# Optimization experiments

Hardware: AMD Instinct MI355X
Metric: run time of the kernel (lower is better)

## Reference

```python
import jax, jax.numpy as jnp
import numpy as np

B, RES, C = 32, 56, 128
HEADS, WS, NW = 4, 7, 8
HD = C // HEADS            # 32
NQ = NW * NW               # 64 windows
WA = WS * WS               # 49 tokens per window
TOPK = 64


def _topk_closest(q_win, k_win, topk):
    qh, qw = q_win; kh, kw = k_win
    ch_q = np.arange(qh); cw_q = np.arange(qw)
    if qh != kh:
        f = kh // qh
        ch_q = ch_q * f + f // 2
        cw_q = cw_q * f + f // 2
    cq = np.stack(np.meshgrid(ch_q, cw_q, indexing='ij'))              # (2,qh,qw)
    ck = np.stack(np.meshgrid(np.arange(kh), np.arange(kw), indexing='ij'))
    fq = cq.reshape(2, -1); fk = ck.reshape(2, -1)
    rel = fq[:, :, None] - fk[:, None, :]                               # (2,nQ,nK)
    dist = np.sqrt(rel[0].astype(np.float32) ** 2 + rel[1].astype(np.float32) ** 2)
    topk = min(topk, dist.shape[1])
    idx = np.argsort(dist, axis=1, kind='stable')[:, :topk]             # (nQ,topk)
    coord = np.take_along_axis(rel, np.broadcast_to(idx[None], (2,) + idx.shape), axis=2)
    return idx.astype(np.int32), coord.transpose(1, 2, 0).astype(np.float32)


def _buffers():
    # window-relative coords, same as register_buffer('window_coords')
    ch = np.arange(WS) - WS // 2
    wc = np.stack(np.meshgrid(ch, ch, indexing='ij'), axis=-1).reshape(-1, 2).astype(np.float32)  # (49,2)
    # level 0: fine grid (RES x RES); level 1: window grid (NW x NW)
    idx0, c0 = _topk_closest((NW, NW), (RES, RES), TOPK)
    idx1, c1 = _topk_closest((NW, NW), (NW, NW), TOPK)
    c1 = c1 * WS  # k > 0 coords scaled by window size
    coords0 = c0[:, None, :, :] + wc[None, :, None, :]   # (NQ,49,TOPK,2)
    coords1 = c1[:, None, :, :] + wc[None, :, None, :]
    return idx0, idx1, coords0, coords1


def setup_inputs() -> dict:
    key = jax.random.key(0)
    ks = jax.random.split(key, 16)
    idx0, idx1, coords0, coords1 = _buffers()
    s = 0.02
    return {
        'x0': jax.random.normal(ks[0], (B, RES, RES, C), jnp.float32),
        'x1': jax.random.normal(ks[1], (B, NQ, C), jnp.float32),
        'qkv_w': jax.random.normal(ks[2], (3 * C, C), jnp.float32) * s,
        'qkv_b': jnp.zeros((3 * C,), jnp.float32),
        'proj_w': jax.random.normal(ks[3], (C, C), jnp.float32) * s,
        'proj_b': jnp.zeros((C,), jnp.float32),
        'rpb0_w1': jax.random.normal(ks[4], (HD, 2), jnp.float32) * s,
        'rpb0_b1': jnp.zeros((HD,), jnp.float32),
        'rpb0_w2': jax.random.normal(ks[5], (HEADS, HD), jnp.float32) * s,
        'rpb0_b2': jnp.zeros((HEADS,), jnp.float32),
        'rpb1_w1': jax.random.normal(ks[6], (HD, 2), jnp.float32) * s,
        'rpb1_b1': jnp.zeros((HD,), jnp.float32),
        'rpb1_w2': jax.random.normal(ks[7], (HEADS, HD), jnp.float32) * s,
        'rpb1_b2': jnp.zeros((HEADS,), jnp.float32),
        'coords0': jnp.asarray(coords0),
        'coords1': jnp.asarray(coords1),
        'idx0': jnp.asarray(idx0),
        'idx1': jnp.asarray(idx1),
    }


def _rpb_mlp(coords, w1, b1, w2, b2):
    # (NQ,49,T,2) -> (NQ,49,T,heads)
    return jax.nn.relu(coords @ w1.T + b1) @ w2.T + b2


def _gather_kv(kv, idx_flat):
    # kv: (B,L,heads,hd); gathered -> (B,NQ,heads,TOPK,hd)
    g = kv[:, idx_flat]
    return g.reshape(kv.shape[0], NQ, TOPK, HEADS, HD).transpose(0, 1, 3, 2, 4)


def reference(x0, x1, qkv_w, qkv_b, proj_w, proj_b,
              rpb0_w1, rpb0_b1, rpb0_w2, rpb0_b2,
              rpb1_w1, rpb1_b1, rpb1_w2, rpb1_b2,
              coords0, coords1, idx0, idx1):
    b = x0.shape[0]
    scale = HD ** -0.5
    qkv = x0 @ qkv_w.T + qkv_b                       # (B,RES,RES,3C)
    q, k, v = jnp.split(qkv, 3, axis=-1)
    # window-partition q: (B,RES,RES,C) -> (B,NQ,heads,49,hd)
    qw = q.reshape(b, NW, WS, NW, WS, C).transpose(0, 1, 3, 2, 4, 5)
    qw = qw.reshape(b, NQ, WA, HEADS, HD).transpose(0, 1, 3, 2, 4)
    # level 0 KV from fine grid
    k0 = k.reshape(b, RES * RES, HEADS, HD)
    v0 = v.reshape(b, RES * RES, HEADS, HD)
    i0 = idx0.reshape(-1)
    k0s, v0s = _gather_kv(k0, i0), _gather_kv(v0, i0)
    # level 1 KV from pooled tokens (same qkv projection)
    qkv1 = (x1 @ qkv_w.T + qkv_b).reshape(b, NQ, 3, HEADS, HD)
    i1 = idx1.reshape(-1)
    k1s, v1s = _gather_kv(qkv1[:, :, 1], i1), _gather_kv(qkv1[:, :, 2], i1)
    k_all = jnp.concatenate([k0s, k1s], axis=3)      # (B,NQ,heads,2T,hd)
    v_all = jnp.concatenate([v0s, v1s], axis=3)
    attn = jnp.einsum('bqhnd,bqhmd->bqhnm', qw * scale, k_all)  # (B,NQ,heads,49,2T)
    rpb0 = _rpb_mlp(coords0, rpb0_w1, rpb0_b1, rpb0_w2, rpb0_b2)
    rpb1 = _rpb_mlp(coords1, rpb1_w1, rpb1_b1, rpb1_w2, rpb1_b2)
    rpb = jnp.concatenate([rpb0, rpb1], axis=2).transpose(0, 3, 1, 2)  # (NQ,heads,49,2T)
    attn = jax.nn.softmax(attn + rpb[None], axis=-1)
    out = jnp.einsum('bqhnm,bqhmd->bqhnd', attn, v_all)
    out = out.transpose(0, 1, 3, 2, 4).reshape(b * NQ, WA, C)
    return out @ proj_w.T + proj_b
```

## Files before the change

kernel.cpp:

```cpp
#include <hip/hip_runtime.h>
#include <hip/hip_bf16.h>


typedef __bf16 bf16_t;
typedef __bf16 bf16x8 __attribute__((ext_vector_type(8)));
typedef float f32x4 __attribute__((ext_vector_type(4)));

static __device__ __forceinline__ f32x4 mfma_bf16(bf16x8 a, bf16x8 b, f32x4 c) {
  return __builtin_amdgcn_mfma_f32_16x16x32_bf16(a, b, c, 0, 0, 0);
}

static __device__ __forceinline__ bf16x8 cvt8(const float* __restrict__ p) {
  float4 a = *(const float4*)p;
  float4 b = *(const float4*)(p + 4);
  bf16x8 r;
  r[0] = (bf16_t)a.x; r[1] = (bf16_t)a.y; r[2] = (bf16_t)a.z; r[3] = (bf16_t)a.w;
  r[4] = (bf16_t)b.x; r[5] = (bf16_t)b.y; r[6] = (bf16_t)b.z; r[7] = (bf16_t)b.w;
  return r;
}

#define NB 32
#define RES 56
#define CH 128
#define NW 8
#define NQ 64
#define WA 49
#define X0_ROWS (NB * RES * RES)
#define SCALE 0.17677669529663687f
#define SQRT32 5.656854249492381f

__global__ __launch_bounds__(256) void k_qkv(
    const float* __restrict__ x0, const float* __restrict__ x1,
    const float* __restrict__ w, const float* __restrict__ bias,
    bf16_t* __restrict__ qout,
    bf16_t* __restrict__ k0, bf16_t* __restrict__ v0,
    bf16_t* __restrict__ k1, bf16_t* __restrict__ v1) {
  __shared__ __align__(16) bf16_t Asm[64][136];
  __shared__ __align__(16) bf16_t Bsm[128][136];
  const int rb = blockIdx.x;
  const int tid = threadIdx.x;
  const size_t row0 = (size_t)rb * 64;
  const bool is_x0 = (rb < 1568);
  const int b_ = rb / 49;
  const int pix0 = (rb - b_ * 49) * 64;
  const int i1base = (rb - 1568) * 64;

  const float* src = is_x0 ? (x0 + row0 * CH)
                           : (x1 + (row0 - X0_ROWS) * CH);
#pragma unroll
  for (int i = 0; i < 4; ++i) {
    int uid = tid + 256 * i;
    int r = uid >> 4, cs = uid & 15;
    *(bf16x8*)&Asm[r][cs * 8] = cvt8(src + (size_t)r * CH + cs * 8);
  }

  const int wid = tid >> 6, l = tid & 63;
  const int lr = l & 15, lkg = l >> 4, lk = lkg * 8;

  for (int cb = 0; cb < 3; ++cb) {
    const float* wsrc = w + (size_t)cb * 128 * CH;
#pragma unroll
    for (int i = 0; i < 8; ++i) {
      int uid = tid + 256 * i;
      int r = uid >> 4, cs = uid & 15;
      *(bf16x8*)&Bsm[r][cs * 8] = cvt8(wsrc + (size_t)r * CH + cs * 8);
    }
    __syncthreads();

    f32x4 zero = {0.f, 0.f, 0.f, 0.f};
    f32x4 acc[8];
#pragma unroll
    for (int nt = 0; nt < 8; ++nt) acc[nt] = zero;
#pragma unroll
    for (int ks = 0; ks < 4; ++ks) {
      bf16x8 a = *(const bf16x8*)&Asm[wid * 16 + lr][ks * 32 + lk];
#pragma unroll
      for (int nt = 0; nt < 8; ++nt) {
        bf16x8 b = *(const bf16x8*)&Bsm[nt * 16 + lr][ks * 32 + lk];
        acc[nt] = mfma_bf16(a, b, acc[nt]);
      }
    }
    float bias_v[8];
#pragma unroll
    for (int nt = 0; nt < 8; ++nt) bias_v[nt] = bias[cb * 128 + nt * 16 + lr];

#pragma unroll
    for (int r4 = 0; r4 < 4; ++r4) {
      int local = wid * 16 + lkg * 4 + r4;
      if (is_x0) {
        int pix = pix0 + local;
        int rr = pix / 56, cc = pix - rr * 56;
        if (cb == 0) {
          int wn = b_ * 64 + (rr / 7) * 8 + cc / 7;
          int nidx = (rr % 7) * 7 + (cc % 7);
          bf16_t* dst = qout + (size_t)wn * 12544 + nidx * 128;
#pragma unroll
          for (int nt = 0; nt < 8; ++nt)
            dst[nt * 16 + lr] = (bf16_t)(acc[nt][r4] + bias_v[nt]);
        } else {
          bf16_t* dst = (cb == 1 ? k0 : v0) +
                        ((size_t)b_ * 3136 + pix) * CH;
#pragma unroll
          for (int nt = 0; nt < 8; ++nt)
            dst[nt * 16 + lr] = (bf16_t)(acc[nt][r4] + bias_v[nt]);
        }
      } else if (cb != 0) {
        bf16_t* dst = (cb == 1 ? k1 : v1) + (size_t)(i1base + local) * CH;
#pragma unroll
        for (int nt = 0; nt < 8; ++nt)
          dst[nt * 16 + lr] = (bf16_t)(acc[nt][r4] + bias_v[nt]);
      }
    }
    __syncthreads();
  }
}

__global__ __launch_bounds__(256) void k_rpb(
    const float* __restrict__ c0, const float* __restrict__ c1,
    const float* __restrict__ w10, const float* __restrict__ b10,
    const float* __restrict__ w20, const float* __restrict__ b20,
    const float* __restrict__ w11, const float* __restrict__ b11,
    const float* __restrict__ w21, const float* __restrict__ b21,
    float* __restrict__ rpb) {
  __shared__ float w1s[2][32][2], b1s[2][32], w2s[2][4][32], b2s[2][4];
  const int tid = threadIdx.x;
  if (tid < 64) {
    int s = tid >> 5, j = tid & 31;
    const float* w1p = s ? w11 : w10;
    const float* b1p = s ? b11 : b10;
    w1s[s][j][0] = w1p[j * 2];
    w1s[s][j][1] = w1p[j * 2 + 1];
    b1s[s][j] = b1p[j];
  }
  {
    int s = tid >> 7, rem = tid & 127, h = rem >> 5, j = rem & 31;
    w2s[s][h][j] = s ? w21[h * 32 + j] : w20[h * 32 + j];
  }
  if (tid < 8) {
    int s = tid >> 2, h = tid & 3;
    b2s[s][h] = s ? b21[h] : b20[h];
  }
  __syncthreads();

  int L = blockIdx.x * 256 + tid;
  int m = L & 127;
  int n = (L >> 7) % WA;
  int qi = L / (128 * WA);
  int s = m >> 6, mi = m & 63;
  const float* cp = (s ? c1 : c0) + (((size_t)qi * WA + n) * 64 + mi) * 2;
  float cx = cp[0], cy = cp[1];
  float a0 = 0.f, a1 = 0.f, a2 = 0.f, a3 = 0.f;
#pragma unroll
  for (int j = 0; j < 32; ++j) {
    float h = fmaxf(w1s[s][j][0] * cx + w1s[s][j][1] * cy + b1s[s][j], 0.f);
    a0 += w2s[s][0][j] * h;
    a1 += w2s[s][1][j] * h;
    a2 += w2s[s][2][j] * h;
    a3 += w2s[s][3][j] * h;
  }
  size_t base = ((size_t)qi * 4 * WA + n) * 128 + m;
  rpb[base] = (a0 + b2s[s][0]) * SQRT32;
  rpb[base + (size_t)WA * 128] = (a1 + b2s[s][1]) * SQRT32;
  rpb[base + (size_t)2 * WA * 128] = (a2 + b2s[s][2]) * SQRT32;
  rpb[base + (size_t)3 * WA * 128] = (a3 + b2s[s][3]) * SQRT32;
}

__global__ __launch_bounds__(256) void k_attn(
    const bf16_t* qin,
    const bf16_t* __restrict__ k0, const bf16_t* __restrict__ v0,
    const bf16_t* __restrict__ k1, const bf16_t* __restrict__ v1,
    const int* __restrict__ idx0, const int* __restrict__ idx1,
    const float* __restrict__ rpb,
    float* attn_out) {
  __shared__ __align__(16) bf16_t Kt[128][72];
  __shared__ __align__(16) bf16_t Vt[64][136];
  __shared__ __align__(16) bf16_t Sm[64][136];

  const int bid = blockIdx.x;
  const int hp = bid & 1;
  const int qi = (bid >> 1) & 63;
  const int b = bid >> 7;
  const int tid = threadIdx.x;
  const int wn = b * 64 + qi;

#pragma unroll
  for (int i = 0; i < 4; ++i) {
    int uid = tid + 256 * i;
    int key = uid & 127, seg = uid >> 7;
    size_t srcrow;
    const bf16_t *kbase, *vbase;
    if (key < 64) {
      srcrow = (size_t)b * 3136 + idx0[qi * 64 + key];
      kbase = k0; vbase = v0;
    } else {
      srcrow = (size_t)b * 64 + idx1[qi * 64 + key - 64];
      kbase = k1; vbase = v1;
    }
    size_t off = srcrow * CH + hp * 64 + seg * 8;
    *(uint4*)&Kt[key][seg * 8] = *(const uint4*)(kbase + off);
    union { uint4 u; bf16_t h[8]; } cv;
    cv.u = *(const uint4*)(vbase + off);
#pragma unroll
    for (int e = 0; e < 8; ++e) Vt[seg * 8 + e][key] = cv.h[e];
  }

  const int wid = tid >> 6, l = tid & 63;
  const int lr = l & 15, lkg = l >> 4, lk = lkg * 8;
  int qr = wid * 16 + lr;
  if (qr > WA - 1) qr = WA - 1;

  const bf16_t* qb = qin + (size_t)wn * 12544;
  bf16x8 qf[2];
  qf[0] = *(const bf16x8*)&qb[qr * 128 + hp * 64 + lk];
  qf[1] = *(const bf16x8*)&qb[qr * 128 + hp * 64 + 32 + lk];
  __syncthreads();

  const int myrow = wid * 16 + lkg * 4;
  float* obase = attn_out + (size_t)wn * 6272;

#pragma unroll
  for (int lh = 0; lh < 2; ++lh) {
    const int hh = hp * 2 + lh;
    const float* rp = rpb + ((size_t)(qi * 4 + hh) * WA) * 128;
    f32x4 acc[8];
#pragma unroll
    for (int nt = 0; nt < 8; ++nt) {
#pragma unroll
      for (int r4 = 0; r4 < 4; ++r4)
        acc[nt][r4] = rp[(myrow + r4) * 128 + nt * 16 + lr];
    }
#pragma unroll
    for (int nt = 0; nt < 8; ++nt) {
      bf16x8 bfr = *(const bf16x8*)&Kt[nt * 16 + lr][lh * 32 + lk];
      acc[nt] = mfma_bf16(qf[lh], bfr, acc[nt]);
    }
    float mx[4] = {-1e30f, -1e30f, -1e30f, -1e30f};
#pragma unroll
    for (int nt = 0; nt < 8; ++nt)
#pragma unroll
      for (int r4 = 0; r4 < 4; ++r4) mx[r4] = fmaxf(mx[r4], acc[nt][r4]);
#pragma unroll
    for (int m = 1; m < 16; m <<= 1)
#pragma unroll
      for (int r4 = 0; r4 < 4; ++r4)
        mx[r4] = fmaxf(mx[r4], __shfl_xor(mx[r4], m));
    float sum[4] = {0.f, 0.f, 0.f, 0.f};
#pragma unroll
    for (int nt = 0; nt < 8; ++nt)
#pragma unroll
      for (int r4 = 0; r4 < 4; ++r4) {
        float p = __expf(SCALE * (acc[nt][r4] - mx[r4]));
        acc[nt][r4] = p;
        sum[r4] += p;
      }
#pragma unroll
    for (int m = 1; m < 16; m <<= 1)
#pragma unroll
      for (int r4 = 0; r4 < 4; ++r4) sum[r4] += __shfl_xor(sum[r4], m);
#pragma unroll
    for (int nt = 0; nt < 8; ++nt)
#pragma unroll
      for (int r4 = 0; r4 < 4; ++r4)
        Sm[myrow + r4][nt * 16 + lr] = (bf16_t)acc[nt][r4];
    f32x4 zero = {0.f, 0.f, 0.f, 0.f};
    f32x4 oacc[2];
    oacc[0] = zero; oacc[1] = zero;
#pragma unroll
    for (int ks = 0; ks < 4; ++ks) {
      bf16x8 pa = *(const bf16x8*)&Sm[wid * 16 + lr][ks * 32 + lk];
#pragma unroll
      for (int nt2 = 0; nt2 < 2; ++nt2) {
        bf16x8 vb = *(const bf16x8*)&Vt[lh * 32 + nt2 * 16 + lr][ks * 32 + lk];
        oacc[nt2] = mfma_bf16(pa, vb, oacc[nt2]);
      }
    }
#pragma unroll
    for (int nt2 = 0; nt2 < 2; ++nt2)
#pragma unroll
      for (int r4 = 0; r4 < 4; ++r4) {
        int rown = myrow + r4;
        if (rown < WA)
          obase[rown * 128 + hh * 32 + nt2 * 16 + lr] = oacc[nt2][r4] / sum[r4];
      }
  }
}

__global__ __launch_bounds__(256) void k_proj(
    const float* attn,
    const float* __restrict__ pw, const float* __restrict__ pb,
    float* out) {
  __shared__ __align__(16) bf16_t Asm[64][136];
  __shared__ __align__(16) bf16_t Bsm[128][136];
  const int rb = blockIdx.x;
  const int tid = threadIdx.x;
  const size_t row0 = (size_t)rb * 64;
#pragma unroll
  for (int i = 0; i < 4; ++i) {
    int uid = tid + 256 * i;
    int r = uid >> 4, cs = uid & 15;
    *(bf16x8*)&Asm[r][cs * 8] = cvt8(attn + (row0 + r) * CH + cs * 8);
  }
#pragma unroll
  for (int i = 0; i < 8; ++i) {
    int uid = tid + 256 * i;
    int r = uid >> 4, cs = uid & 15;
    *(bf16x8*)&Bsm[r][cs * 8] = cvt8(pw + (size_t)r * CH + cs * 8);
  }
  __syncthreads();

  const int wid = tid >> 6, l = tid & 63;
  const int lr = l & 15, lkg = l >> 4, lk = lkg * 8;
  f32x4 zero = {0.f, 0.f, 0.f, 0.f};
  f32x4 acc[8];
#pragma unroll
  for (int nt = 0; nt < 8; ++nt) acc[nt] = zero;
#pragma unroll
  for (int ks = 0; ks < 4; ++ks) {
    bf16x8 a = *(const bf16x8*)&Asm[wid * 16 + lr][ks * 32 + lk];
#pragma unroll
    for (int nt = 0; nt < 8; ++nt) {
      bf16x8 b = *(const bf16x8*)&Bsm[nt * 16 + lr][ks * 32 + lk];
      acc[nt] = mfma_bf16(a, b, acc[nt]);
    }
  }
#pragma unroll
  for (int nt = 0; nt < 8; ++nt) {
    int n = nt * 16 + lr;
    float bs = pb[n];
#pragma unroll
    for (int r4 = 0; r4 < 4; ++r4) {
      size_t g = row0 + (size_t)(wid * 16 + lkg * 4 + r4);
      out[g * CH + n] = acc[nt][r4] + bs;
    }
  }
}

extern "C" void kernel_launch(void* const* d_in, const int* in_sizes, int n_in,
                              void* d_out, int out_size, void* d_ws, size_t ws_size,
                              hipStream_t stream) {
  const float* x0 = (const float*)d_in[0];
  const float* x1 = (const float*)d_in[1];
  const float* qkv_w = (const float*)d_in[2];
  const float* qkv_b = (const float*)d_in[3];
  const float* proj_w = (const float*)d_in[4];
  const float* proj_b = (const float*)d_in[5];
  const float* rpb0_w1 = (const float*)d_in[6];
  const float* rpb0_b1 = (const float*)d_in[7];
  const float* rpb0_w2 = (const float*)d_in[8];
  const float* rpb0_b2 = (const float*)d_in[9];
  const float* rpb1_w1 = (const float*)d_in[10];
  const float* rpb1_b1 = (const float*)d_in[11];
  const float* rpb1_w2 = (const float*)d_in[12];
  const float* rpb1_b2 = (const float*)d_in[13];
  const float* coords0 = (const float*)d_in[14];
  const float* coords1 = (const float*)d_in[15];
  const int* idx0 = (const int*)d_in[16];
  const int* idx1 = (const int*)d_in[17];

  char* ws = (char*)d_ws;
  bf16_t* k0 = (bf16_t*)(ws + 0);
  bf16_t* v0 = (bf16_t*)(ws + 25690112);
  bf16_t* k1 = (bf16_t*)(ws + 51380224);
  bf16_t* v1 = (bf16_t*)(ws + 51904512);
  float* rpb = (float*)(ws + 52428800);

  k_qkv<<<1600, 256, 0, stream>>>(x0, x1, qkv_w, qkv_b,
                                  (bf16_t*)d_out, k0, v0, k1, v1);
  k_rpb<<<1568, 256, 0, stream>>>(coords0, coords1, rpb0_w1, rpb0_b1, rpb0_w2,
                                  rpb0_b2, rpb1_w1, rpb1_b1, rpb1_w2, rpb1_b2,
                                  rpb);
  k_attn<<<4096, 256, 0, stream>>>((const bf16_t*)d_out, k0, v0, k1, v1,
                                   idx0, idx1, rpb, (float*)d_out);
  k_proj<<<1568, 256, 0, stream>>>((const float*)d_out, proj_w, proj_b,
                                   (float*)d_out);
}
```

Baseline: 227.4 us.

## Stage GEMM outputs through LDS for coalesced stores, store rpb as bf16

The qkv and proj kernels now keep the A operand in registers and reuse the freed shared-memory tile to stage the output, so global writes become 16-byte coalesced stores instead of scattered 2- or 4-byte ones. The rpb table is stored as bf16 in a transposed layout that the attention kernel prefetches into registers with vector loads. The softmax now uses exp2 with a pre-folded scale and a reciprocal multiply. Launch bounds gain an occupancy hint. Storing rpb in bf16 lowers its precision, and the extra barriers add some synchronisation cost.

```diff
diff --git a/kernel.cpp b/kernel.cpp
--- a/kernel.cpp
+++ b/kernel.cpp
@@ -4,6 +4,7 @@
 
 typedef __bf16 bf16_t;
 typedef __bf16 bf16x8 __attribute__((ext_vector_type(8)));
+typedef __bf16 bf16x4 __attribute__((ext_vector_type(4)));
 typedef float f32x4 __attribute__((ext_vector_type(4)));
 
 static __device__ __forceinline__ f32x4 mfma_bf16(bf16x8 a, bf16x8 b, f32x4 c) {
@@ -28,34 +29,34 @@
 #define X0_ROWS (NB * RES * RES)
 #define SCALE 0.17677669529663687f
 #define SQRT32 5.656854249492381f
-
-__global__ __launch_bounds__(256) void k_qkv(
+#define KE 0.25503164508761f
+
+__global__ __launch_bounds__(256, 4) void k_qkv(
     const float* __restrict__ x0, const float* __restrict__ x1,
     const float* __restrict__ w, const float* __restrict__ bias,
     bf16_t* __restrict__ qout,
     bf16_t* __restrict__ k0, bf16_t* __restrict__ v0,
     bf16_t* __restrict__ k1, bf16_t* __restrict__ v1) {
-  __shared__ __align__(16) bf16_t Asm[64][136];
   __shared__ __align__(16) bf16_t Bsm[128][136];
+  bf16_t (*Csm)[136] = (bf16_t(*)[136])&Bsm[0][0];
+
   const int rb = blockIdx.x;
   const int tid = threadIdx.x;
   const size_t row0 = (size_t)rb * 64;
   const bool is_x0 = (rb < 1568);
   const int b_ = rb / 49;
   const int pix0 = (rb - b_ * 49) * 64;
-  const int i1base = (rb - 1568) * 64;
-
-  const float* src = is_x0 ? (x0 + row0 * CH)
-                           : (x1 + (row0 - X0_ROWS) * CH);
-#pragma unroll
-  for (int i = 0; i < 4; ++i) {
-    int uid = tid + 256 * i;
-    int r = uid >> 4, cs = uid & 15;
-    *(bf16x8*)&Asm[r][cs * 8] = cvt8(src + (size_t)r * CH + cs * 8);
-  }
+  const int i1base = (int)(row0 - (size_t)X0_ROWS);
 
   const int wid = tid >> 6, l = tid & 63;
   const int lr = l & 15, lkg = l >> 4, lk = lkg * 8;
+  const int myrow = wid * 16 + lkg * 4;
+
+  const float* src = is_x0 ? (x0 + row0 * CH) : (x1 + (size_t)i1base * CH);
+  bf16x8 aA[4];
+#pragma unroll
+  for (int ks = 0; ks < 4; ++ks)
+    aA[ks] = cvt8(src + (size_t)(wid * 16 + lr) * CH + ks * 32 + lk);
 
   for (int cb = 0; cb < 3; ++cb) {
     const float* wsrc = w + (size_t)cb * 128 * CH;
@@ -73,45 +74,54 @@
     for (int nt = 0; nt < 8; ++nt) acc[nt] = zero;
 #pragma unroll
     for (int ks = 0; ks < 4; ++ks) {
-      bf16x8 a = *(const bf16x8*)&Asm[wid * 16 + lr][ks * 32 + lk];
 #pragma unroll
       for (int nt = 0; nt < 8; ++nt) {
         bf16x8 b = *(const bf16x8*)&Bsm[nt * 16 + lr][ks * 32 + lk];
-        acc[nt] = mfma_bf16(a, b, acc[nt]);
+        acc[nt] = mfma_bf16(aA[ks], b, acc[nt]);
       }
     }
-    float bias_v[8];
-#pragma unroll
-    for (int nt = 0; nt < 8; ++nt) bias_v[nt] = bias[cb * 128 + nt * 16 + lr];
-
-#pragma unroll
-    for (int r4 = 0; r4 < 4; ++r4) {
-      int local = wid * 16 + lkg * 4 + r4;
-      if (is_x0) {
-        int pix = pix0 + local;
-        int rr = pix / 56, cc = pix - rr * 56;
-        if (cb == 0) {
+    __syncthreads();
+
+    const bool emit = is_x0 || (cb != 0);
+    if (emit) {
+      float bias_v[8];
+#pragma unroll
+      for (int nt = 0; nt < 8; ++nt) bias_v[nt] = bias[cb * 128 + nt * 16 + lr];
+#pragma unroll
+      for (int nt = 0; nt < 8; ++nt)
+#pragma unroll
+        for (int r4 = 0; r4 < 4; ++r4)
+          Csm[myrow + r4][nt * 16 + lr] = (bf16_t)(acc[nt][r4] + bias_v[nt]);
+      __syncthreads();
+
+      if (cb == 0) {
+#pragma unroll
+        for (int i = 0; i < 4; ++i) {
+          int uid = tid + 256 * i;
+          int r = uid >> 4, cs = uid & 15;
+          int pix = pix0 + r;
+          int rr = pix / 56, cc = pix - rr * 56;
           int wn = b_ * 64 + (rr / 7) * 8 + cc / 7;
           int nidx = (rr % 7) * 7 + (cc % 7);
-          bf16_t* dst = qout + (size_t)wn * 12544 + nidx * 128;
-#pragma unroll
-          for (int nt = 0; nt < 8; ++nt)
-            dst[nt * 16 + lr] = (bf16_t)(acc[nt][r4] + bias_v[nt]);
-        } else {
-          bf16_t* dst = (cb == 1 ? k0 : v0) +
-                        ((size_t)b_ * 3136 + pix) * CH;
-#pragma unroll
-          for (int nt = 0; nt < 8; ++nt)
-            dst[nt * 16 + lr] = (bf16_t)(acc[nt][r4] + bias_v[nt]);
+          *(uint4*)(qout + (size_t)wn * 12544 + nidx * 128 + cs * 8) =
+              *(const uint4*)&Csm[r][cs * 8];
         }
-      } else if (cb != 0) {
-        bf16_t* dst = (cb == 1 ? k1 : v1) + (size_t)(i1base + local) * CH;
-#pragma unroll
-        for (int nt = 0; nt < 8; ++nt)
-          dst[nt * 16 + lr] = (bf16_t)(acc[nt][r4] + bias_v[nt]);
+      } else {
+        bf16_t* dst;
+        if (is_x0)
+          dst = (cb == 1 ? k0 : v0) + ((size_t)b_ * 3136 + pix0) * CH;
+        else
+          dst = (cb == 1 ? k1 : v1) + (size_t)i1base * CH;
+#pragma unroll
+        for (int i = 0; i < 4; ++i) {
+          int uid = tid + 256 * i;
+          int r = uid >> 4, cs = uid & 15;
+          *(uint4*)(dst + (size_t)r * CH + cs * 8) =
+              *(const uint4*)&Csm[r][cs * 8];
+        }
       }
-    }
-    __syncthreads();
+      __syncthreads();
+    }
   }
 }
 
@@ -121,7 +131,7 @@
     const float* __restrict__ w20, const float* __restrict__ b20,
     const float* __restrict__ w11, const float* __restrict__ b11,
     const float* __restrict__ w21, const float* __restrict__ b21,
-    float* __restrict__ rpb) {
+    bf16_t* __restrict__ rpb) {
   __shared__ float w1s[2][32][2], b1s[2][32], w2s[2][4][32], b2s[2][4];
   const int tid = threadIdx.x;
   if (tid < 64) {
@@ -142,12 +152,13 @@
   }
   __syncthreads();
 
-  int L = blockIdx.x * 256 + tid;
-  int m = L & 127;
-  int n = (L >> 7) % WA;
-  int qi = L / (128 * WA);
-  int s = m >> 6, mi = m & 63;
-  const float* cp = (s ? c1 : c0) + (((size_t)qi * WA + n) * 64 + mi) * 2;
+  const int bid = blockIdx.x;
+  const int qi = bid >> 5;
+  const int m = ((bid & 31) << 2) | (tid >> 6);
+  const int n = tid & 63;
+  const int nc = (n < WA) ? n : (WA - 1);
+  const int s = m >> 6, mi = m & 63;
+  const float* cp = (s ? c1 : c0) + (((size_t)qi * WA + nc) * 64 + mi) * 2;
   float cx = cp[0], cy = cp[1];
   float a0 = 0.f, a1 = 0.f, a2 = 0.f, a3 = 0.f;
 #pragma unroll
@@ -158,11 +169,11 @@
     a2 += w2s[s][2][j] * h;
     a3 += w2s[s][3][j] * h;
   }
-  size_t base = ((size_t)qi * 4 * WA + n) * 128 + m;
-  rpb[base] = (a0 + b2s[s][0]) * SQRT32;
-  rpb[base + (size_t)WA * 128] = (a1 + b2s[s][1]) * SQRT32;
-  rpb[base + (size_t)2 * WA * 128] = (a2 + b2s[s][2]) * SQRT32;
-  rpb[base + (size_t)3 * WA * 128] = (a3 + b2s[s][3]) * SQRT32;
+  size_t base = ((size_t)(qi * 4) * 128 + m) * 64 + n;
+  rpb[base]         = (bf16_t)((a0 + b2s[s][0]) * SQRT32);
+  rpb[base + 8192]  = (bf16_t)((a1 + b2s[s][1]) * SQRT32);
+  rpb[base + 16384] = (bf16_t)((a2 + b2s[s][2]) * SQRT32);
+  rpb[base + 24576] = (bf16_t)((a3 + b2s[s][3]) * SQRT32);
 }
 
 __global__ __launch_bounds__(256) void k_attn(
@@ -170,7 +181,7 @@
     const bf16_t* __restrict__ k0, const bf16_t* __restrict__ v0,
     const bf16_t* __restrict__ k1, const bf16_t* __restrict__ v1,
     const int* __restrict__ idx0, const int* __restrict__ idx1,
-    const float* __restrict__ rpb,
+    const bf16_t* __restrict__ rpb,
     float* attn_out) {
   __shared__ __align__(16) bf16_t Kt[128][72];
   __shared__ __align__(16) bf16_t Vt[64][136];
@@ -206,6 +217,7 @@
 
   const int wid = tid >> 6, l = tid & 63;
   const int lr = l & 15, lkg = l >> 4, lk = lkg * 8;
+  const int myrow = wid * 16 + lkg * 4;
   int qr = wid * 16 + lr;
   if (qr > WA - 1) qr = WA - 1;
 
@@ -213,22 +225,28 @@
   bf16x8 qf[2];
   qf[0] = *(const bf16x8*)&qb[qr * 128 + hp * 64 + lk];
   qf[1] = *(const bf16x8*)&qb[qr * 128 + hp * 64 + 32 + lk];
+
+  const bf16_t* rbase = rpb + (size_t)(qi * 4 + hp * 2) * 8192;
+  bf16x4 rpre[2][8];
+#pragma unroll
+  for (int lh = 0; lh < 2; ++lh)
+#pragma unroll
+    for (int nt = 0; nt < 8; ++nt)
+      rpre[lh][nt] =
+          *(const bf16x4*)&rbase[((size_t)lh * 128 + nt * 16 + lr) * 64 + myrow];
+
   __syncthreads();
 
-  const int myrow = wid * 16 + lkg * 4;
   float* obase = attn_out + (size_t)wn * 6272;
 
 #pragma unroll
   for (int lh = 0; lh < 2; ++lh) {
     const int hh = hp * 2 + lh;
-    const float* rp = rpb + ((size_t)(qi * 4 + hh) * WA) * 128;
     f32x4 acc[8];
 #pragma unroll
-    for (int nt = 0; nt < 8; ++nt) {
-#pragma unroll
-      for (int r4 = 0; r4 < 4; ++r4)
-        acc[nt][r4] = rp[(myrow + r4) * 128 + nt * 16 + lr];
-    }
+    for (int nt = 0; nt < 8; ++nt)
+#pragma unroll
+      for (int r4 = 0; r4 < 4; ++r4) acc[nt][r4] = (float)rpre[lh][nt][r4];
 #pragma unroll
     for (int nt = 0; nt < 8; ++nt) {
       bf16x8 bfr = *(const bf16x8*)&Kt[nt * 16 + lr][lh * 32 + lk];
@@ -244,12 +262,15 @@
 #pragma unroll
       for (int r4 = 0; r4 < 4; ++r4)
         mx[r4] = fmaxf(mx[r4], __shfl_xor(mx[r4], m));
+    float km[4];
+#pragma unroll
+    for (int r4 = 0; r4 < 4; ++r4) km[r4] = KE * mx[r4];
     float sum[4] = {0.f, 0.f, 0.f, 0.f};
 #pragma unroll
     for (int nt = 0; nt < 8; ++nt)
 #pragma unroll
       for (int r4 = 0; r4 < 4; ++r4) {
-        float p = __expf(SCALE * (acc[nt][r4] - mx[r4]));
+        float p = __builtin_amdgcn_exp2f(fmaf(KE, acc[nt][r4], -km[r4]));
         acc[nt][r4] = p;
         sum[r4] += p;
       }
@@ -257,6 +278,9 @@
     for (int m = 1; m < 16; m <<= 1)
 #pragma unroll
       for (int r4 = 0; r4 < 4; ++r4) sum[r4] += __shfl_xor(sum[r4], m);
+    float inv[4];
+#pragma unroll
+    for (int r4 = 0; r4 < 4; ++r4) inv[r4] = __builtin_amdgcn_rcpf(sum[r4]);
 #pragma unroll
     for (int nt = 0; nt < 8; ++nt)
 #pragma unroll
@@ -280,26 +304,29 @@
       for (int r4 = 0; r4 < 4; ++r4) {
         int rown = myrow + r4;
         if (rown < WA)
-          obase[rown * 128 + hh * 32 + nt2 * 16 + lr] = oacc[nt2][r4] / sum[r4];
+          obase[rown * 128 + hh * 32 + nt2 * 16 + lr] = oacc[nt2][r4] * inv[r4];
       }
   }
 }
 
-__global__ __launch_bounds__(256) void k_proj(
+__global__ __launch_bounds__(256, 4) void k_proj(
     const float* attn,
     const float* __restrict__ pw, const float* __restrict__ pb,
     float* out) {
-  __shared__ __align__(16) bf16_t Asm[64][136];
   __shared__ __align__(16) bf16_t Bsm[128][136];
+  float (*Csm)[136] = (float(*)[136])&Bsm[0][0];
+
   const int rb = blockIdx.x;
   const int tid = threadIdx.x;
   const size_t row0 = (size_t)rb * 64;
-#pragma unroll
-  for (int i = 0; i < 4; ++i) {
-    int uid = tid + 256 * i;
-    int r = uid >> 4, cs = uid & 15;
-    *(bf16x8*)&Asm[r][cs * 8] = cvt8(attn + (row0 + r) * CH + cs * 8);
-  }
+  const int wid = tid >> 6, l = tid & 63;
+  const int lr = l & 15, lkg = l >> 4, lk = lkg * 8;
+  const int myrow = wid * 16 + lkg * 4;
+
+  bf16x8 aA[4];
+#pragma unroll
+  for (int ks = 0; ks < 4; ++ks)
+    aA[ks] = cvt8(attn + (row0 + wid * 16 + lr) * CH + ks * 32 + lk);
 #pragma unroll
   for (int i = 0; i < 8; ++i) {
     int uid = tid + 256 * i;
@@ -308,30 +335,35 @@
   }
   __syncthreads();
 
-  const int wid = tid >> 6, l = tid & 63;
-  const int lr = l & 15, lkg = l >> 4, lk = lkg * 8;
   f32x4 zero = {0.f, 0.f, 0.f, 0.f};
   f32x4 acc[8];
 #pragma unroll
   for (int nt = 0; nt < 8; ++nt) acc[nt] = zero;
 #pragma unroll
   for (int ks = 0; ks < 4; ++ks) {
-    bf16x8 a = *(const bf16x8*)&Asm[wid * 16 + lr][ks * 32 + lk];
 #pragma unroll
     for (int nt = 0; nt < 8; ++nt) {
       bf16x8 b = *(const bf16x8*)&Bsm[nt * 16 + lr][ks * 32 + lk];
-      acc[nt] = mfma_bf16(a, b, acc[nt]);
-    }
-  }
-#pragma unroll
-  for (int nt = 0; nt < 8; ++nt) {
-    int n = nt * 16 + lr;
-    float bs = pb[n];
-#pragma unroll
-    for (int r4 = 0; r4 < 4; ++r4) {
-      size_t g = row0 + (size_t)(wid * 16 + lkg * 4 + r4);
-      out[g * CH + n] = acc[nt][r4] + bs;
-    }
+      acc[nt] = mfma_bf16(aA[ks], b, acc[nt]);
+    }
+  }
+  __syncthreads();
+
+  float bias_v[8];
+#pragma unroll
+  for (int nt = 0; nt < 8; ++nt) bias_v[nt] = pb[nt * 16 + lr];
+#pragma unroll
+  for (int nt = 0; nt < 8; ++nt)
+#pragma unroll
+    for (int r4 = 0; r4 < 4; ++r4)
+      Csm[myrow + r4][nt * 16 + lr] = acc[nt][r4] + bias_v[nt];
+  __syncthreads();
+
+#pragma unroll
+  for (int i = 0; i < 8; ++i) {
+    int uid = tid + 256 * i;
+    int r = uid >> 5, cs = uid & 31;
+    *(float4*)(out + (row0 + r) * CH + cs * 4) = *(const float4*)&Csm[r][cs * 4];
   }
 }
 
@@ -362,11 +394,11 @@
   bf16_t* v0 = (bf16_t*)(ws + 25690112);
   bf16_t* k1 = (bf16_t*)(ws + 51380224);
   bf16_t* v1 = (bf16_t*)(ws + 51904512);
-  float* rpb = (float*)(ws + 52428800);
+  bf16_t* rpb = (bf16_t*)(ws + 52428800);
 
   k_qkv<<<1600, 256, 0, stream>>>(x0, x1, qkv_w, qkv_b,
                                   (bf16_t*)d_out, k0, v0, k1, v1);
-  k_rpb<<<1568, 256, 0, stream>>>(coords0, coords1, rpb0_w1, rpb0_b1, rpb0_w2,
+  k_rpb<<<2048, 256, 0, stream>>>(coords0, coords1, rpb0_w1, rpb0_b1, rpb0_w2,
                                   rpb0_b2, rpb1_w1, rpb1_b1, rpb1_w2, rpb1_b2,
                                   rpb);
   k_attn<<<4096, 256, 0, stream>>>((const bf16_t*)d_out, k0, v0, k1, v1,
```

Measured after the change: 248.5 us. +9.3%, slower.
